# Performance work log

Measured on AMD Instinct MI355X. Metric: run time of the kernel, lower is better.

The kernel has to match this reference:

```python
import jax, jax.numpy as jnp
import numpy as np

B, SORB, H, L = 32768, 64, 256, 2


def setup_inputs() -> dict:
    key = jax.random.key(0)
    ks = jax.random.split(key, 11)
    s = 1.0 / np.sqrt(H)

    def u(k, shape):
        return jax.random.uniform(k, shape, jnp.float32, -s, s)

    return {
        "x": jax.random.randint(ks[0], (B, SORB), 0, 2).astype(jnp.int32),
        # PyTorch GRU params, gate order (r, z, n); layer 0 input_size=2, layer 1 input_size=H
        "w_ih0": u(ks[1], (3 * H, 2)), "w_hh0": u(ks[2], (3 * H, H)),
        "b_ih0": u(ks[3], (3 * H,)), "b_hh0": u(ks[4], (3 * H,)),
        "w_ih1": u(ks[5], (3 * H, H)), "w_hh1": u(ks[6], (3 * H, H)),
        "b_ih1": u(ks[7], (3 * H,)), "b_hh1": u(ks[8], (3 * H,)),
        "w_amp": u(ks[9], (2, H)), "b_amp": u(ks[10], (2,)),
    }


def _gru_cell(x, h, w_ih, w_hh, b_ih, b_hh):
    # PyTorch GRUCell math, gates in (r, z, n) order
    gi = x @ w_ih.T + b_ih
    gh = h @ w_hh.T + b_hh
    ir, iz, i_n = jnp.split(gi, 3, axis=-1)
    hr, hz, h_n = jnp.split(gh, 3, axis=-1)
    r = jax.nn.sigmoid(ir + hr)
    z = jax.nn.sigmoid(iz + hz)
    n = jnp.tanh(i_n + r * h_n)
    return (1.0 - z) * n + z * h


def reference(x, w_ih0, w_hh0, b_ih0, b_hh0, w_ih1, w_hh1, b_ih1, b_hh1, w_amp, b_amp):
    bits = x  # [B, SORB], values in {0,1} (equals ((+-1)+1)/2 of original input)
    nb = bits.shape[0]
    layer_params = [(w_ih0, w_hh0, b_ih0, b_hh0), (w_ih1, w_hh1, b_ih1, b_hh1)]

    def stacked(inp, h):  # h: [L, B, H]
        hs = []
        for l, (wi, wh, bi, bh) in enumerate(layer_params):
            hl = _gru_cell(inp, h[l], wi, wh, bi, bh)
            hs.append(hl)
            inp = hl
        return inp, jnp.stack(hs)

    h0 = jnp.zeros((L, nb, H), jnp.float32)
    # priming step with zero input (x0 = zeros(nbatch,1,2))
    _, h = stacked(jnp.zeros((nb, 2), jnp.float32), h0)

    def step(h, b_t):  # b_t: [B]
        onehot = jax.nn.one_hot(b_t, 2, dtype=jnp.float32)
        y, h = stacked(onehot, h)
        amp = jax.nn.softmax(y @ w_amp.T + b_amp, axis=1)  # [B, 2]
        p = jnp.sum(amp * onehot, axis=1)  # conditional prob of the sampled bit
        return h, p

    _, probs = jax.lax.scan(step, h, bits.T)  # probs: [SORB, B]
    return jnp.sqrt(jnp.prod(probs, axis=0))  # wavefunction amplitude, [B]
```

## Files before the change

### kernel.cpp

```cpp
#include <hip/hip_runtime.h>

typedef _Float16 f16;
typedef _Float16 f16x8 __attribute__((ext_vector_type(8)));
typedef float f32x4 __attribute__((ext_vector_type(4)));

#define H_    256
#define TB_   64
#define NT_   1024
#define SORB_ 64
#define SLOT_ 8192

#define MFMA16(a, b, c) __builtin_amdgcn_mfma_f32_16x16x32_f16((a), (b), (c), 0, 0, 0)
#define UNR _Pragma("unroll")

__device__ __forceinline__ float sigm(float v) {
  return __builtin_amdgcn_rcpf(1.0f + __builtin_amdgcn_exp2f(v * -1.442695040888963f));
}
__device__ __forceinline__ float tanh_fast(float v) {
  float a = fabsf(v);
  float e = __builtin_amdgcn_exp2f(a * -2.885390081777927f);
  float t = (1.0f - e) * __builtin_amdgcn_rcpf(1.0f + e);
  return copysignf(t, v);
}
__device__ __forceinline__ int lswz(int lrow, int col) {
  return lrow * H_ + (col ^ ((lrow & 7) << 3));
}

__global__ void wcvt(const float* __restrict__ a, const float* __restrict__ b,
                     const float* __restrict__ c, f16* __restrict__ o) {
  int i = blockIdx.x * 256 + threadIdx.x;
  const int n = 768 * 256;
  if (i < n) {
    o[i]         = (f16)a[i];
    o[n + i]     = (f16)b[i];
    o[2 * n + i] = (f16)c[i];
  }
}

__global__ __launch_bounds__(NT_, 4) void rnnwf(
    const int* __restrict__ x,
    const float* __restrict__ w_ih0, const float* __restrict__ b_ih0,
    const float* __restrict__ b_hh0, const float* __restrict__ b_ih1,
    const float* __restrict__ b_hh1, const float* __restrict__ w_amp,
    const float* __restrict__ b_amp, const f16* __restrict__ W16,
    float* __restrict__ out)
{
  __shared__ __align__(16) f16 hall[6 * SLOT_];
  __shared__ float wampL[512];
  __shared__ unsigned short bitsL[TB_ * 4];
  __shared__ unsigned long long bitsT[SORB_];

  const int tid  = threadIdx.x;
  const int wave = tid >> 6;
  const int lane = tid & 63;
  const int l15  = lane & 15;
  const int lg   = lane >> 4;
  const int lg4  = lg << 2;
  const int col  = wave * 16 + l15;
  const int rowbase = blockIdx.x * TB_;

  for (int j = tid; j < 512; j += NT_) wampL[j] = w_amp[j];
  if (tid < 256) {
    int row = tid >> 2, q = tid & 3;
    const int* xp = x + (size_t)(rowbase + row) * SORB_ + q * 16;
    unsigned m = 0;
    #pragma unroll
    for (int i = 0; i < 16; ++i) m |= (unsigned)(xp[i] & 1) << i;
    bitsL[row * 4 + q] = (unsigned short)m;
  }
  for (int i = tid; i < 6 * SLOT_; i += NT_) hall[i] = (f16)0.f;

  const float baseR = b_ih0[col]       + b_hh0[col];
  const float baseZ = b_ih0[256 + col] + b_hh0[256 + col];
  const float baseN = b_ih0[512 + col];
  const float wR0 = w_ih0[2 * col + 0],         wR1 = w_ih0[2 * col + 1];
  const float wZ0 = w_ih0[2 * (256 + col) + 0], wZ1 = w_ih0[2 * (256 + col) + 1];
  const float wN0 = w_ih0[2 * (512 + col) + 0], wN1 = w_ih0[2 * (512 + col) + 1];
  const float sumR0 = baseR + wR0, dR = wR1 - wR0;
  const float sumZ0 = baseZ + wZ0, dZ = wZ1 - wZ0;
  const float sumN0 = baseN + wN0, dN = wN1 - wN0;
  const float bhh0n_c = b_hh0[512 + col];
  const float b1r_c   = b_ih1[col]       + b_hh1[col];
  const float b1z_c   = b_ih1[256 + col] + b_hh1[256 + col];
  const float b1ni_c  = b_ih1[512 + col];
  const float b1nh_c  = b_hh1[512 + col];
  const float ba0 = b_amp[0], ba1 = b_amp[1];
  __syncthreads();

  if (tid < SORB_) {
    unsigned long long mk = 0ull;
    const int q = tid >> 4, sh = tid & 15;
    #pragma unroll 4
    for (int r = 0; r < TB_; ++r)
      mk |= (unsigned long long)((bitsL[r * 4 + q] >> sh) & 1) << r;
    bitsT[tid] = mk;
  }
  __syncthreads();

  float prob = 1.0f;
  const f16* Wih1 = W16 + 768 * 256;
  const f16* Whh1 = W16 + 2 * 768 * 256;
  const f16* p0base = W16  + col * 256;
  const f16* pibase = Wih1 + col * 256;
  const f16* phbase = Whh1 + col * 256;

  const int hrow = tid >> 4;
  const int hsh  = hrow & 31;
  const bool hhi = hrow >= 32;

  int pa = 0, pb = 2 * SLOT_, pc = 4 * SLOT_;

  for (int t = -1; t < SORB_; ++t) {
    unsigned lo32 = 0u, hi32 = 0u;
    if (t >= 0) {
      unsigned long long mk = bitsT[t];
      lo32 = (unsigned)mk; hi32 = (unsigned)(mk >> 32);
    }

    {
      f32x4 aR[4], aZ[4], aN[4];
      UNR for (int m = 0; m < 4; ++m) { aR[m] = (f32x4){0,0,0,0}; aZ[m] = aR[m]; aN[m] = aR[m]; }
      #pragma unroll 2
      for (int kt = 0; kt < 8; ++kt) {
        const int k0 = kt * 32 + lg * 8;
        f16x8 Br = *(const f16x8*)(p0base + k0);
        f16x8 Bz = *(const f16x8*)(p0base + 65536 + k0);
        f16x8 Bn = *(const f16x8*)(p0base + 131072 + k0);
        UNR for (int m = 0; m < 4; ++m) {
          f16x8 A = *(const f16x8*)&hall[pa + (m >> 1) * SLOT_ + lswz((m & 1) * 16 + l15, k0)];
          aR[m] = MFMA16(A, Br, aR[m]);
          aZ[m] = MFMA16(A, Bz, aZ[m]);
          aN[m] = MFMA16(A, Bn, aN[m]);
        }
      }
      if (t >= 0) {
        UNR for (int m = 0; m < 4; ++m) {
          const unsigned hsel = (m < 2) ? lo32 : hi32;
          UNR for (int e = 0; e < 4; ++e) {
            const int lrow = (m & 1) * 16 + lg4 + e;
            float fb = (float)((hsel >> ((m & 1) * 16 + lg4 + e)) & 1u);
            float giR = fmaf(fb, dR, sumR0);
            float giZ = fmaf(fb, dZ, sumZ0);
            float giN = fmaf(fb, dN, sumN0);
            float r  = sigm(aR[m][e] + giR);
            float z  = sigm(aZ[m][e] + giZ);
            float n  = tanh_fast(giN + r * (aN[m][e] + bhh0n_c));
            float ho = (float)hall[pa + (m >> 1) * SLOT_ + lswz(lrow, col)];
            hall[pc + (m >> 1) * SLOT_ + lswz(lrow, col)] = (f16)((1.0f - z) * n + z * ho);
          }
        }
      } else {
        UNR for (int m = 0; m < 4; ++m) {
          UNR for (int e = 0; e < 4; ++e) {
            const int lrow = (m & 1) * 16 + lg4 + e;
            float r  = sigm(aR[m][e] + baseR);
            float z  = sigm(aZ[m][e] + baseZ);
            float n  = tanh_fast(baseN + r * (aN[m][e] + bhh0n_c));
            float ho = (float)hall[pa + (m >> 1) * SLOT_ + lswz(lrow, col)];
            hall[pc + (m >> 1) * SLOT_ + lswz(lrow, col)] = (f16)((1.0f - z) * n + z * ho);
          }
        }
      }
    }
    __syncthreads();

    {
      f32x4 aR[4], aZ[4];
      UNR for (int m = 0; m < 4; ++m) { aR[m] = (f32x4){0,0,0,0}; aZ[m] = aR[m]; }
      #pragma unroll 2
      for (int kt = 0; kt < 8; ++kt) {
        const int k0 = kt * 32 + lg * 8;
        f16x8 BiR = *(const f16x8*)(pibase + k0);
        f16x8 BiZ = *(const f16x8*)(pibase + 65536 + k0);
        f16x8 BhR = *(const f16x8*)(phbase + k0);
        f16x8 BhZ = *(const f16x8*)(phbase + 65536 + k0);
        UNR for (int m = 0; m < 4; ++m) {
          f16x8 A0 = *(const f16x8*)&hall[pc + (m >> 1) * SLOT_ + lswz((m & 1) * 16 + l15, k0)];
          f16x8 A1 = *(const f16x8*)&hall[pb + (m >> 1) * SLOT_ + lswz((m & 1) * 16 + l15, k0)];
          aR[m] = MFMA16(A0, BiR, aR[m]);  aR[m] = MFMA16(A1, BhR, aR[m]);
          aZ[m] = MFMA16(A0, BiZ, aZ[m]);  aZ[m] = MFMA16(A1, BhZ, aZ[m]);
        }
      }
      f32x4 rv[4], zv[4];
      UNR for (int m = 0; m < 4; ++m)
        UNR for (int e = 0; e < 4; ++e) {
          rv[m][e] = sigm(aR[m][e] + b1r_c);
          zv[m][e] = sigm(aZ[m][e] + b1z_c);
        }
      f32x4 aNi[4], aNh[4];
      UNR for (int m = 0; m < 4; ++m) { aNi[m] = (f32x4){0,0,0,0}; aNh[m] = aNi[m]; }
      #pragma unroll 2
      for (int kt = 0; kt < 8; ++kt) {
        const int k0 = kt * 32 + lg * 8;
        f16x8 BiN = *(const f16x8*)(pibase + 131072 + k0);
        f16x8 BhN = *(const f16x8*)(phbase + 131072 + k0);
        UNR for (int m = 0; m < 4; ++m) {
          f16x8 A0 = *(const f16x8*)&hall[pc + (m >> 1) * SLOT_ + lswz((m & 1) * 16 + l15, k0)];
          f16x8 A1 = *(const f16x8*)&hall[pb + (m >> 1) * SLOT_ + lswz((m & 1) * 16 + l15, k0)];
          aNi[m] = MFMA16(A0, BiN, aNi[m]);
          aNh[m] = MFMA16(A1, BhN, aNh[m]);
        }
      }
      UNR for (int m = 0; m < 4; ++m) {
        UNR for (int e = 0; e < 4; ++e) {
          const int lrow = (m & 1) * 16 + lg4 + e;
          float n  = tanh_fast(aNi[m][e] + b1ni_c + rv[m][e] * (aNh[m][e] + b1nh_c));
          float z  = zv[m][e];
          float ho = (float)hall[pb + (m >> 1) * SLOT_ + lswz(lrow, col)];
          hall[pa + (m >> 1) * SLOT_ + lswz(lrow, col)] = (f16)((1.0f - z) * n + z * ho);
        }
      }
    }
    __syncthreads();

    if (t >= 0) {
      const int t16 = tid & 15;
      float d0 = 0.f, d1 = 0.f;
      #pragma unroll
      for (int j = 0; j < 2; ++j) {
        const int k0 = t16 * 16 + j * 8;
        f16x8 hv = *(const f16x8*)&hall[pa + (hrow >> 5) * SLOT_ + lswz(hrow & 31, k0)];
        f32x4 w0a = *(const f32x4*)&wampL[k0];
        f32x4 w0b = *(const f32x4*)&wampL[k0 + 4];
        f32x4 w1a = *(const f32x4*)&wampL[256 + k0];
        f32x4 w1b = *(const f32x4*)&wampL[256 + k0 + 4];
        #pragma unroll
        for (int i = 0; i < 4; ++i) {
          float hfa = (float)hv[i], hfb = (float)hv[4 + i];
          d0 = fmaf(hfa, w0a[i], d0); d0 = fmaf(hfb, w0b[i], d0);
          d1 = fmaf(hfa, w1a[i], d1); d1 = fmaf(hfb, w1b[i], d1);
        }
      }
      d0 += __shfl_xor(d0, 1); d0 += __shfl_xor(d0, 2);
      d0 += __shfl_xor(d0, 4); d0 += __shfl_xor(d0, 8);
      d1 += __shfl_xor(d1, 1); d1 += __shfl_xor(d1, 2);
      d1 += __shfl_xor(d1, 4); d1 += __shfl_xor(d1, 8);
      const unsigned hm = hhi ? hi32 : lo32;
      const int bit = (hm >> hsh) & 1;
      float diff = (d0 + ba0) - (d1 + ba1);
      if (bit) diff = -diff;
      prob *= __builtin_amdgcn_rcpf(1.0f + __builtin_amdgcn_exp2f(diff * -1.442695040888963f));
    }

    int tmp = pa; pa = pc; pc = pb; pb = tmp;
  }

  if ((tid & 15) == 0) out[rowbase + (tid >> 4)] = sqrtf(prob);
}

extern "C" void kernel_launch(void* const* d_in, const int* in_sizes, int n_in,
                              void* d_out, int out_size, void* d_ws, size_t ws_size,
                              hipStream_t stream) {
  const int*   x     = (const int*)d_in[0];
  const float* w_ih0 = (const float*)d_in[1];
  const float* w_hh0 = (const float*)d_in[2];
  const float* b_ih0 = (const float*)d_in[3];
  const float* b_hh0 = (const float*)d_in[4];
  const float* w_ih1 = (const float*)d_in[5];
  const float* w_hh1 = (const float*)d_in[6];
  const float* b_ih1 = (const float*)d_in[7];
  const float* b_hh1 = (const float*)d_in[8];
  const float* w_amp = (const float*)d_in[9];
  const float* b_amp = (const float*)d_in[10];
  (void)in_sizes; (void)n_in; (void)out_size; (void)ws_size;

  f16* W16 = (f16*)d_ws;
  hipLaunchKernelGGL(wcvt, dim3(768), dim3(256), 0, stream, w_hh0, w_ih1, w_hh1, W16);
  hipLaunchKernelGGL(rnnwf, dim3(32768 / TB_), dim3(NT_), 0, stream,
                     x, w_ih0, b_ih0, b_hh0, b_ih1, b_hh1, w_amp, b_amp, W16,
                     (float*)d_out);
}
```

Baseline: 5.107 ms.

## Halve rows per block and have each wave compute two column tiles

Cuts the batch tile from 64 to 32 rows and the block from 1024 to 512 threads, so each wave now handles two 16-column tiles (col and col+128) over 32 rows instead of one tile over 64 rows. Hidden-state LDS shrinks by half, and the per-row bit masks are now held in registers, read straight from packed shorts, instead of being transposed into a shared bitsT table. The aim is more resident blocks per CU and smaller LDS and sync scope. In exchange each B-fragment of the weights is reused across fewer A-rows, which doubles global or L2 weight traffic per row.

```diff
diff --git a/kernel.cpp b/kernel.cpp
--- a/kernel.cpp
+++ b/kernel.cpp
@@ -5,8 +5,9 @@
 typedef float f32x4 __attribute__((ext_vector_type(4)));
 
 #define H_    256
-#define TB_   64
-#define NT_   1024
+#define TB_   32
+#define NT_   512
+#define NWG_  1024
 #define SORB_ 64
 #define SLOT_ 8192
 
@@ -45,10 +46,8 @@
     const float* __restrict__ b_amp, const f16* __restrict__ W16,
     float* __restrict__ out)
 {
-  __shared__ __align__(16) f16 hall[6 * SLOT_];
+  __shared__ __align__(16) f16 hall[3 * SLOT_];
   __shared__ float wampL[512];
-  __shared__ unsigned short bitsL[TB_ * 4];
-  __shared__ unsigned long long bitsT[SORB_];
 
   const int tid  = threadIdx.x;
   const int wave = tid >> 6;
@@ -56,170 +55,164 @@
   const int l15  = lane & 15;
   const int lg   = lane >> 4;
   const int lg4  = lg << 2;
-  const int col  = wave * 16 + l15;
+  const int colA = wave * 16 + l15;
+  const int colB = colA + 128;
   const int rowbase = blockIdx.x * TB_;
 
   for (int j = tid; j < 512; j += NT_) wampL[j] = w_amp[j];
-  if (tid < 256) {
-    int row = tid >> 2, q = tid & 3;
-    const int* xp = x + (size_t)(rowbase + row) * SORB_ + q * 16;
+  if (tid < TB_ * 4) {
+    const int* xp = x + (size_t)(rowbase + (tid >> 2)) * SORB_ + (tid & 3) * 16;
     unsigned m = 0;
     #pragma unroll
     for (int i = 0; i < 16; ++i) m |= (unsigned)(xp[i] & 1) << i;
-    bitsL[row * 4 + q] = (unsigned short)m;
-  }
-  for (int i = tid; i < 6 * SLOT_; i += NT_) hall[i] = (f16)0.f;
-
-  const float baseR = b_ih0[col]       + b_hh0[col];
-  const float baseZ = b_ih0[256 + col] + b_hh0[256 + col];
-  const float baseN = b_ih0[512 + col];
-  const float wR0 = w_ih0[2 * col + 0],         wR1 = w_ih0[2 * col + 1];
-  const float wZ0 = w_ih0[2 * (256 + col) + 0], wZ1 = w_ih0[2 * (256 + col) + 1];
-  const float wN0 = w_ih0[2 * (512 + col) + 0], wN1 = w_ih0[2 * (512 + col) + 1];
-  const float sumR0 = baseR + wR0, dR = wR1 - wR0;
-  const float sumZ0 = baseZ + wZ0, dZ = wZ1 - wZ0;
-  const float sumN0 = baseN + wN0, dN = wN1 - wN0;
-  const float bhh0n_c = b_hh0[512 + col];
-  const float b1r_c   = b_ih1[col]       + b_hh1[col];
-  const float b1z_c   = b_ih1[256 + col] + b_hh1[256 + col];
-  const float b1ni_c  = b_ih1[512 + col];
-  const float b1nh_c  = b_hh1[512 + col];
+    ((unsigned short*)hall)[tid] = (unsigned short)m;
+  }
+  __syncthreads();
+  unsigned long long mk[8];
+  UNR for (int m = 0; m < 2; ++m)
+    UNR for (int e = 0; e < 4; ++e)
+      mk[m * 4 + e] = ((const unsigned long long*)hall)[m * 16 + lg4 + e];
+  const unsigned long long hmk = ((const unsigned long long*)hall)[tid >> 4];
+  __syncthreads();
+  for (int i = tid; i < 3 * SLOT_; i += NT_) hall[i] = (f16)0.f;
+
+  float sumR0[2], dR[2], sumZ0[2], dZ[2], sumN0[2], dN[2], bhh0n_c[2];
+  float b1r_c[2], b1z_c[2], b1ni_c[2], b1nh_c[2];
+  UNR for (int nt = 0; nt < 2; ++nt) {
+    const int c = nt ? colB : colA;
+    const float baseR = b_ih0[c] + b_hh0[c];
+    const float baseZ = b_ih0[256 + c] + b_hh0[256 + c];
+    const float baseN = b_ih0[512 + c];
+    sumR0[nt] = baseR + w_ih0[2 * c + 0];           dR[nt] = w_ih0[2 * c + 1] - w_ih0[2 * c + 0];
+    sumZ0[nt] = baseZ + w_ih0[2 * (256 + c) + 0];   dZ[nt] = w_ih0[2 * (256 + c) + 1] - w_ih0[2 * (256 + c) + 0];
+    sumN0[nt] = baseN + w_ih0[2 * (512 + c) + 0];   dN[nt] = w_ih0[2 * (512 + c) + 1] - w_ih0[2 * (512 + c) + 0];
+    bhh0n_c[nt] = b_hh0[512 + c];
+    b1r_c[nt]  = b_ih1[c] + b_hh1[c];
+    b1z_c[nt]  = b_ih1[256 + c] + b_hh1[256 + c];
+    b1ni_c[nt] = b_ih1[512 + c];
+    b1nh_c[nt] = b_hh1[512 + c];
+  }
   const float ba0 = b_amp[0], ba1 = b_amp[1];
-  __syncthreads();
-
-  if (tid < SORB_) {
-    unsigned long long mk = 0ull;
-    const int q = tid >> 4, sh = tid & 15;
-    #pragma unroll 4
-    for (int r = 0; r < TB_; ++r)
-      mk |= (unsigned long long)((bitsL[r * 4 + q] >> sh) & 1) << r;
-    bitsT[tid] = mk;
-  }
   __syncthreads();
 
   float prob = 1.0f;
   const f16* Wih1 = W16 + 768 * 256;
   const f16* Whh1 = W16 + 2 * 768 * 256;
-  const f16* p0base = W16  + col * 256;
-  const f16* pibase = Wih1 + col * 256;
-  const f16* phbase = Whh1 + col * 256;
-
   const int hrow = tid >> 4;
-  const int hsh  = hrow & 31;
-  const bool hhi = hrow >= 32;
-
-  int pa = 0, pb = 2 * SLOT_, pc = 4 * SLOT_;
+  const int t16  = tid & 15;
+
+  int pa = 0, pb = SLOT_, pc = 2 * SLOT_;
 
   for (int t = -1; t < SORB_; ++t) {
-    unsigned lo32 = 0u, hi32 = 0u;
-    if (t >= 0) {
-      unsigned long long mk = bitsT[t];
-      lo32 = (unsigned)mk; hi32 = (unsigned)(mk >> 32);
-    }
-
-    {
-      f32x4 aR[4], aZ[4], aN[4];
-      UNR for (int m = 0; m < 4; ++m) { aR[m] = (f32x4){0,0,0,0}; aZ[m] = aR[m]; aN[m] = aR[m]; }
+    UNR for (int nt = 0; nt < 2; ++nt) {
+      const int c = nt ? colB : colA;
+      const f16* p0 = W16 + c * 256;
+      f32x4 aR[2], aZ[2], aN[2];
+      UNR for (int m = 0; m < 2; ++m) { aR[m] = (f32x4){0,0,0,0}; aZ[m] = aR[m]; aN[m] = aR[m]; }
       #pragma unroll 2
       for (int kt = 0; kt < 8; ++kt) {
         const int k0 = kt * 32 + lg * 8;
-        f16x8 Br = *(const f16x8*)(p0base + k0);
-        f16x8 Bz = *(const f16x8*)(p0base + 65536 + k0);
-        f16x8 Bn = *(const f16x8*)(p0base + 131072 + k0);
-        UNR for (int m = 0; m < 4; ++m) {
-          f16x8 A = *(const f16x8*)&hall[pa + (m >> 1) * SLOT_ + lswz((m & 1) * 16 + l15, k0)];
+        f16x8 Br = *(const f16x8*)(p0 + k0);
+        f16x8 Bz = *(const f16x8*)(p0 + 65536 + k0);
+        f16x8 Bn = *(const f16x8*)(p0 + 131072 + k0);
+        UNR for (int m = 0; m < 2; ++m) {
+          f16x8 A = *(const f16x8*)&hall[pa + lswz(m * 16 + l15, k0)];
           aR[m] = MFMA16(A, Br, aR[m]);
           aZ[m] = MFMA16(A, Bz, aZ[m]);
           aN[m] = MFMA16(A, Bn, aN[m]);
         }
       }
       if (t >= 0) {
-        UNR for (int m = 0; m < 4; ++m) {
-          const unsigned hsel = (m < 2) ? lo32 : hi32;
+        UNR for (int m = 0; m < 2; ++m) {
           UNR for (int e = 0; e < 4; ++e) {
-            const int lrow = (m & 1) * 16 + lg4 + e;
-            float fb = (float)((hsel >> ((m & 1) * 16 + lg4 + e)) & 1u);
-            float giR = fmaf(fb, dR, sumR0);
-            float giZ = fmaf(fb, dZ, sumZ0);
-            float giN = fmaf(fb, dN, sumN0);
+            const int lrow = m * 16 + lg4 + e;
+            float fb = (float)((unsigned)(mk[m * 4 + e] >> t) & 1u);
+            float giR = fmaf(fb, dR[nt], sumR0[nt]);
+            float giZ = fmaf(fb, dZ[nt], sumZ0[nt]);
+            float giN = fmaf(fb, dN[nt], sumN0[nt]);
             float r  = sigm(aR[m][e] + giR);
             float z  = sigm(aZ[m][e] + giZ);
-            float n  = tanh_fast(giN + r * (aN[m][e] + bhh0n_c));
-            float ho = (float)hall[pa + (m >> 1) * SLOT_ + lswz(lrow, col)];
-            hall[pc + (m >> 1) * SLOT_ + lswz(lrow, col)] = (f16)((1.0f - z) * n + z * ho);
+            float n  = tanh_fast(giN + r * (aN[m][e] + bhh0n_c[nt]));
+            float ho = (float)hall[pa + lswz(lrow, c)];
+            hall[pc + lswz(lrow, c)] = (f16)((1.0f - z) * n + z * ho);
           }
         }
       } else {
-        UNR for (int m = 0; m < 4; ++m) {
+        const float pR = b_ih0[c] + b_hh0[c];
+        const float pZ = b_ih0[256 + c] + b_hh0[256 + c];
+        const float pN = b_ih0[512 + c];
+        UNR for (int m = 0; m < 2; ++m) {
           UNR for (int e = 0; e < 4; ++e) {
-            const int lrow = (m & 1) * 16 + lg4 + e;
-            float r  = sigm(aR[m][e] + baseR);
-            float z  = sigm(aZ[m][e] + baseZ);
-            float n  = tanh_fast(baseN + r * (aN[m][e] + bhh0n_c));
-            float ho = (float)hall[pa + (m >> 1) * SLOT_ + lswz(lrow, col)];
-            hall[pc + (m >> 1) * SLOT_ + lswz(lrow, col)] = (f16)((1.0f - z) * n + z * ho);
+            const int lrow = m * 16 + lg4 + e;
+            float r  = sigm(aR[m][e] + pR);
+            float z  = sigm(aZ[m][e] + pZ);
+            float n  = tanh_fast(pN + r * (aN[m][e] + bhh0n_c[nt]));
+            float ho = (float)hall[pa + lswz(lrow, c)];
+            hall[pc + lswz(lrow, c)] = (f16)((1.0f - z) * n + z * ho);
           }
         }
       }
     }
     __syncthreads();
 
-    {
-      f32x4 aR[4], aZ[4];
-      UNR for (int m = 0; m < 4; ++m) { aR[m] = (f32x4){0,0,0,0}; aZ[m] = aR[m]; }
+    UNR for (int nt = 0; nt < 2; ++nt) {
+      const int c = nt ? colB : colA;
+      const f16* pi = Wih1 + c * 256;
+      const f16* ph = Whh1 + c * 256;
+      f32x4 aR[2], aZ[2];
+      UNR for (int m = 0; m < 2; ++m) { aR[m] = (f32x4){0,0,0,0}; aZ[m] = aR[m]; }
       #pragma unroll 2
       for (int kt = 0; kt < 8; ++kt) {
         const int k0 = kt * 32 + lg * 8;
-        f16x8 BiR = *(const f16x8*)(pibase + k0);
-        f16x8 BiZ = *(const f16x8*)(pibase + 65536 + k0);
-        f16x8 BhR = *(const f16x8*)(phbase + k0);
-        f16x8 BhZ = *(const f16x8*)(phbase + 65536 + k0);
-        UNR for (int m = 0; m < 4; ++m) {
-          f16x8 A0 = *(const f16x8*)&hall[pc + (m >> 1) * SLOT_ + lswz((m & 1) * 16 + l15, k0)];
-          f16x8 A1 = *(const f16x8*)&hall[pb + (m >> 1) * SLOT_ + lswz((m & 1) * 16 + l15, k0)];
+        f16x8 BiR = *(const f16x8*)(pi + k0);
+        f16x8 BiZ = *(const f16x8*)(pi + 65536 + k0);
+        f16x8 BhR = *(const f16x8*)(ph + k0);
+        f16x8 BhZ = *(const f16x8*)(ph + 65536 + k0);
+        UNR for (int m = 0; m < 2; ++m) {
+          f16x8 A0 = *(const f16x8*)&hall[pc + lswz(m * 16 + l15, k0)];
+          f16x8 A1 = *(const f16x8*)&hall[pb + lswz(m * 16 + l15, k0)];
           aR[m] = MFMA16(A0, BiR, aR[m]);  aR[m] = MFMA16(A1, BhR, aR[m]);
           aZ[m] = MFMA16(A0, BiZ, aZ[m]);  aZ[m] = MFMA16(A1, BhZ, aZ[m]);
         }
       }
-      f32x4 rv[4], zv[4];
-      UNR for (int m = 0; m < 4; ++m)
+      f32x4 rv[2], zv[2];
+      UNR for (int m = 0; m < 2; ++m)
         UNR for (int e = 0; e < 4; ++e) {
-          rv[m][e] = sigm(aR[m][e] + b1r_c);
-          zv[m][e] = sigm(aZ[m][e] + b1z_c);
-        }
-      f32x4 aNi[4], aNh[4];
-      UNR for (int m = 0; m < 4; ++m) { aNi[m] = (f32x4){0,0,0,0}; aNh[m] = aNi[m]; }
+          rv[m][e] = sigm(aR[m][e] + b1r_c[nt]);
+          zv[m][e] = sigm(aZ[m][e] + b1z_c[nt]);
+        }
+      f32x4 aNi[2], aNh[2];
+      UNR for (int m = 0; m < 2; ++m) { aNi[m] = (f32x4){0,0,0,0}; aNh[m] = aNi[m]; }
       #pragma unroll 2
       for (int kt = 0; kt < 8; ++kt) {
         const int k0 = kt * 32 + lg * 8;
-        f16x8 BiN = *(const f16x8*)(pibase + 131072 + k0);
-        f16x8 BhN = *(const f16x8*)(phbase + 131072 + k0);
-        UNR for (int m = 0; m < 4; ++m) {
-          f16x8 A0 = *(const f16x8*)&hall[pc + (m >> 1) * SLOT_ + lswz((m & 1) * 16 + l15, k0)];
-          f16x8 A1 = *(const f16x8*)&hall[pb + (m >> 1) * SLOT_ + lswz((m & 1) * 16 + l15, k0)];
+        f16x8 BiN = *(const f16x8*)(pi + 131072 + k0);
+        f16x8 BhN = *(const f16x8*)(ph + 131072 + k0);
+        UNR for (int m = 0; m < 2; ++m) {
+          f16x8 A0 = *(const f16x8*)&hall[pc + lswz(m * 16 + l15, k0)];
+          f16x8 A1 = *(const f16x8*)&hall[pb + lswz(m * 16 + l15, k0)];
           aNi[m] = MFMA16(A0, BiN, aNi[m]);
           aNh[m] = MFMA16(A1, BhN, aNh[m]);
         }
       }
-      UNR for (int m = 0; m < 4; ++m) {
+      UNR for (int m = 0; m < 2; ++m) {
         UNR for (int e = 0; e < 4; ++e) {
-          const int lrow = (m & 1) * 16 + lg4 + e;
-          float n  = tanh_fast(aNi[m][e] + b1ni_c + rv[m][e] * (aNh[m][e] + b1nh_c));
+          const int lrow = m * 16 + lg4 + e;
+          float n  = tanh_fast(aNi[m][e] + b1ni_c[nt] + rv[m][e] * (aNh[m][e] + b1nh_c[nt]));
           float z  = zv[m][e];
-          float ho = (float)hall[pb + (m >> 1) * SLOT_ + lswz(lrow, col)];
-          hall[pa + (m >> 1) * SLOT_ + lswz(lrow, col)] = (f16)((1.0f - z) * n + z * ho);
+          float ho = (float)hall[pb + lswz(lrow, c)];
+          hall[pa + lswz(lrow, c)] = (f16)((1.0f - z) * n + z * ho);
         }
       }
     }
     __syncthreads();
 
     if (t >= 0) {
-      const int t16 = tid & 15;
       float d0 = 0.f, d1 = 0.f;
       #pragma unroll
       for (int j = 0; j < 2; ++j) {
         const int k0 = t16 * 16 + j * 8;
-        f16x8 hv = *(const f16x8*)&hall[pa + (hrow >> 5) * SLOT_ + lswz(hrow & 31, k0)];
+        f16x8 hv = *(const f16x8*)&hall[pa + lswz(hrow, k0)];
         f32x4 w0a = *(const f32x4*)&wampL[k0];
         f32x4 w0b = *(const f32x4*)&wampL[k0 + 4];
         f32x4 w1a = *(const f32x4*)&wampL[256 + k0];
@@ -235,8 +228,7 @@
       d0 += __shfl_xor(d0, 4); d0 += __shfl_xor(d0, 8);
       d1 += __shfl_xor(d1, 1); d1 += __shfl_xor(d1, 2);
       d1 += __shfl_xor(d1, 4); d1 += __shfl_xor(d1, 8);
-      const unsigned hm = hhi ? hi32 : lo32;
-      const int bit = (hm >> hsh) & 1;
+      const int bit = (unsigned)(hmk >> t) & 1u;
       float diff = (d0 + ba0) - (d1 + ba1);
       if (bit) diff = -diff;
       prob *= __builtin_amdgcn_rcpf(1.0f + __builtin_amdgcn_exp2f(diff * -1.442695040888963f));
@@ -245,7 +237,7 @@
     int tmp = pa; pa = pc; pc = pb; pb = tmp;
   }
 
-  if ((tid & 15) == 0) out[rowbase + (tid >> 4)] = sqrtf(prob);
+  if (t16 == 0) out[rowbase + hrow] = sqrtf(prob);
 }
 
 extern "C" void kernel_launch(void* const* d_in, const int* in_sizes, int n_in,
@@ -266,7 +258,7 @@
 
   f16* W16 = (f16*)d_ws;
   hipLaunchKernelGGL(wcvt, dim3(768), dim3(256), 0, stream, w_hh0, w_ih1, w_hh1, W16);
-  hipLaunchKernelGGL(rnnwf, dim3(32768 / TB_), dim3(NT_), 0, stream,
+  hipLaunchKernelGGL(rnnwf, dim3(NWG_), dim3(NT_), 0, stream,
                      x, w_ih0, b_ih0, b_hh0, b_ih1, b_hh1, w_amp, b_amp, W16,
                      (float*)d_out);
 }
```

After: 8.445 ms. 1.65x slower.

## Software-pipeline GRU layers across timesteps with one barrier per step

Applied to the files above, without the earlier changes.

Restructures the time loop so that layer 0 at step tau and layer 1 at step tau-1 run in the same iteration, each reading double-buffered hidden states. The amplitude softmax for step tau-2 is folded in as well, and the shared A0 fragment is loaded once for both layer-0 gates and layer-1 input gates. This cuts the barriers per step from two to one and interleaves independent MFMA work. In exchange it grows LDS to eight slots, which may lower occupancy, and adds an epilogue iteration for the final step.

```diff
diff --git a/kernel.cpp b/kernel.cpp
--- a/kernel.cpp
+++ b/kernel.cpp
@@ -45,9 +45,9 @@
     const float* __restrict__ b_amp, const f16* __restrict__ W16,
     float* __restrict__ out)
 {
-  __shared__ __align__(16) f16 hall[6 * SLOT_];
+  __shared__ __align__(16) f16 hall[8 * SLOT_];
   __shared__ float wampL[512];
-  __shared__ unsigned short bitsL[TB_ * 4];
+  __shared__ __align__(8) unsigned short bitsL[TB_ * 4];
   __shared__ unsigned long long bitsT[SORB_];
 
   const int tid  = threadIdx.x;
@@ -60,25 +60,33 @@
   const int rowbase = blockIdx.x * TB_;
 
   for (int j = tid; j < 512; j += NT_) wampL[j] = w_amp[j];
-  if (tid < 256) {
-    int row = tid >> 2, q = tid & 3;
-    const int* xp = x + (size_t)(rowbase + row) * SORB_ + q * 16;
+  if (tid < TB_ * 4) {
+    const int* xp = x + (size_t)(rowbase + (tid >> 2)) * SORB_ + (tid & 3) * 16;
     unsigned m = 0;
     #pragma unroll
     for (int i = 0; i < 16; ++i) m |= (unsigned)(xp[i] & 1) << i;
-    bitsL[row * 4 + q] = (unsigned short)m;
-  }
-  for (int i = tid; i < 6 * SLOT_; i += NT_) hall[i] = (f16)0.f;
+    bitsL[tid] = (unsigned short)m;
+  }
+  for (int i = tid; i < 8 * SLOT_; i += NT_) hall[i] = (f16)0.f;
+  __syncthreads();
+  if (tid < SORB_) {
+    unsigned long long mkk = 0ull;
+    const int q = tid >> 4, sh = tid & 15;
+    #pragma unroll 4
+    for (int r = 0; r < TB_; ++r)
+      mkk |= (unsigned long long)((bitsL[r * 4 + q] >> sh) & 1) << r;
+    bitsT[tid] = mkk;
+  }
+  const int hrow = tid >> 4;
+  const int t16  = tid & 15;
+  const unsigned long long hmk = ((const unsigned long long*)bitsL)[hrow];
 
   const float baseR = b_ih0[col]       + b_hh0[col];
   const float baseZ = b_ih0[256 + col] + b_hh0[256 + col];
   const float baseN = b_ih0[512 + col];
-  const float wR0 = w_ih0[2 * col + 0],         wR1 = w_ih0[2 * col + 1];
-  const float wZ0 = w_ih0[2 * (256 + col) + 0], wZ1 = w_ih0[2 * (256 + col) + 1];
-  const float wN0 = w_ih0[2 * (512 + col) + 0], wN1 = w_ih0[2 * (512 + col) + 1];
-  const float sumR0 = baseR + wR0, dR = wR1 - wR0;
-  const float sumZ0 = baseZ + wZ0, dZ = wZ1 - wZ0;
-  const float sumN0 = baseN + wN0, dN = wN1 - wN0;
+  const float sumR0 = baseR + w_ih0[2 * col + 0],         dR = w_ih0[2 * col + 1] - w_ih0[2 * col + 0];
+  const float sumZ0 = baseZ + w_ih0[2 * (256 + col) + 0], dZ = w_ih0[2 * (256 + col) + 1] - w_ih0[2 * (256 + col) + 0];
+  const float sumN0 = baseN + w_ih0[2 * (512 + col) + 0], dN = w_ih0[2 * (512 + col) + 1] - w_ih0[2 * (512 + col) + 0];
   const float bhh0n_c = b_hh0[512 + col];
   const float b1r_c   = b_ih1[col]       + b_hh1[col];
   const float b1z_c   = b_ih1[256 + col] + b_hh1[256 + col];
@@ -87,53 +95,87 @@
   const float ba0 = b_amp[0], ba1 = b_amp[1];
   __syncthreads();
 
-  if (tid < SORB_) {
-    unsigned long long mk = 0ull;
-    const int q = tid >> 4, sh = tid & 15;
-    #pragma unroll 4
-    for (int r = 0; r < TB_; ++r)
-      mk |= (unsigned long long)((bitsL[r * 4 + q] >> sh) & 1) << r;
-    bitsT[tid] = mk;
-  }
-  __syncthreads();
-
   float prob = 1.0f;
-  const f16* Wih1 = W16 + 768 * 256;
-  const f16* Whh1 = W16 + 2 * 768 * 256;
-  const f16* p0base = W16  + col * 256;
-  const f16* pibase = Wih1 + col * 256;
-  const f16* phbase = Whh1 + col * 256;
-
-  const int hrow = tid >> 4;
-  const int hsh  = hrow & 31;
-  const bool hhi = hrow >= 32;
-
-  int pa = 0, pb = 2 * SLOT_, pc = 4 * SLOT_;
-
-  for (int t = -1; t < SORB_; ++t) {
+  const f16* p0base = W16 + col * 256;
+  const f16* pibase = W16 + 768 * 256 + col * 256;
+  const f16* phbase = W16 + 2 * 768 * 256 + col * 256;
+
+  for (int tau = -1; tau <= 64; ++tau) {
+    const int h0r = ((tau + 1) & 1) * (2 * SLOT_);
+    const int h0w = (tau & 1) * (2 * SLOT_);
+    const int h1r = 4 * SLOT_ + ((tau + 1) & 1) * (2 * SLOT_);
+    const int h1w = 4 * SLOT_ + (tau & 1) * (2 * SLOT_);
+    const bool doS = (tau < 64), doT = (tau >= 0);
+
     unsigned lo32 = 0u, hi32 = 0u;
-    if (t >= 0) {
-      unsigned long long mk = bitsT[t];
-      lo32 = (unsigned)mk; hi32 = (unsigned)(mk >> 32);
-    }
-
-    {
-      f32x4 aR[4], aZ[4], aN[4];
-      UNR for (int m = 0; m < 4; ++m) { aR[m] = (f32x4){0,0,0,0}; aZ[m] = aR[m]; aN[m] = aR[m]; }
+    if (tau >= 0 && tau < 64) {
+      unsigned long long mkk = bitsT[tau];
+      lo32 = (unsigned)mkk; hi32 = (unsigned)(mkk >> 32);
+    }
+
+    f32x4 aR0[4], aZ0[4], aN0[4], tR[4], tZ[4];
+    UNR for (int m = 0; m < 4; ++m) {
+      aR0[m] = (f32x4){0,0,0,0}; aZ0[m] = aR0[m]; aN0[m] = aR0[m];
+      tR[m] = aR0[m]; tZ[m] = aR0[m];
+    }
+    #pragma unroll 2
+    for (int kt = 0; kt < 8; ++kt) {
+      const int k0 = kt * 32 + lg * 8;
+      f16x8 A0[4];
+      UNR for (int m = 0; m < 4; ++m)
+        A0[m] = *(const f16x8*)&hall[h0r + (m >> 1) * SLOT_ + lswz((m & 1) * 16 + l15, k0)];
+      if (doS) {
+        f16x8 Br = *(const f16x8*)(p0base + k0);
+        f16x8 Bz = *(const f16x8*)(p0base + 65536 + k0);
+        f16x8 Bn = *(const f16x8*)(p0base + 131072 + k0);
+        UNR for (int m = 0; m < 4; ++m) {
+          aR0[m] = MFMA16(A0[m], Br, aR0[m]);
+          aZ0[m] = MFMA16(A0[m], Bz, aZ0[m]);
+          aN0[m] = MFMA16(A0[m], Bn, aN0[m]);
+        }
+      }
+      if (doT) {
+        f16x8 BiR = *(const f16x8*)(pibase + k0);
+        f16x8 BiZ = *(const f16x8*)(pibase + 65536 + k0);
+        f16x8 BhR = *(const f16x8*)(phbase + k0);
+        f16x8 BhZ = *(const f16x8*)(phbase + 65536 + k0);
+        f16x8 A1[4];
+        UNR for (int m = 0; m < 4; ++m)
+          A1[m] = *(const f16x8*)&hall[h1r + (m >> 1) * SLOT_ + lswz((m & 1) * 16 + l15, k0)];
+        UNR for (int m = 0; m < 4; ++m) {
+          tR[m] = MFMA16(A0[m], BiR, tR[m]);  tR[m] = MFMA16(A1[m], BhR, tR[m]);
+          tZ[m] = MFMA16(A0[m], BiZ, tZ[m]);  tZ[m] = MFMA16(A1[m], BhZ, tZ[m]);
+        }
+      }
+    }
+    f32x4 rv[4], zv[4];
+    if (doT) {
+      UNR for (int m = 0; m < 4; ++m)
+        UNR for (int e = 0; e < 4; ++e) {
+          rv[m][e] = sigm(tR[m][e] + b1r_c);
+          zv[m][e] = sigm(tZ[m][e] + b1z_c);
+        }
+    }
+
+    f32x4 tNi[4], tNh[4];
+    UNR for (int m = 0; m < 4; ++m) { tNi[m] = (f32x4){0,0,0,0}; tNh[m] = tNi[m]; }
+    if (doT) {
       #pragma unroll 2
       for (int kt = 0; kt < 8; ++kt) {
         const int k0 = kt * 32 + lg * 8;
-        f16x8 Br = *(const f16x8*)(p0base + k0);
-        f16x8 Bz = *(const f16x8*)(p0base + 65536 + k0);
-        f16x8 Bn = *(const f16x8*)(p0base + 131072 + k0);
-        UNR for (int m = 0; m < 4; ++m) {
-          f16x8 A = *(const f16x8*)&hall[pa + (m >> 1) * SLOT_ + lswz((m & 1) * 16 + l15, k0)];
-          aR[m] = MFMA16(A, Br, aR[m]);
-          aZ[m] = MFMA16(A, Bz, aZ[m]);
-          aN[m] = MFMA16(A, Bn, aN[m]);
-        }
-      }
-      if (t >= 0) {
+        f16x8 BiN = *(const f16x8*)(pibase + 131072 + k0);
+        f16x8 BhN = *(const f16x8*)(phbase + 131072 + k0);
+        UNR for (int m = 0; m < 4; ++m) {
+          f16x8 A0 = *(const f16x8*)&hall[h0r + (m >> 1) * SLOT_ + lswz((m & 1) * 16 + l15, k0)];
+          f16x8 A1 = *(const f16x8*)&hall[h1r + (m >> 1) * SLOT_ + lswz((m & 1) * 16 + l15, k0)];
+          tNi[m] = MFMA16(A0, BiN, tNi[m]);
+          tNh[m] = MFMA16(A1, BhN, tNh[m]);
+        }
+      }
+    }
+
+    if (doS) {
+      if (tau >= 0) {
         UNR for (int m = 0; m < 4; ++m) {
           const unsigned hsel = (m < 2) ? lo32 : hi32;
           UNR for (int e = 0; e < 4; ++e) {
@@ -142,84 +184,44 @@
             float giR = fmaf(fb, dR, sumR0);
             float giZ = fmaf(fb, dZ, sumZ0);
             float giN = fmaf(fb, dN, sumN0);
-            float r  = sigm(aR[m][e] + giR);
-            float z  = sigm(aZ[m][e] + giZ);
-            float n  = tanh_fast(giN + r * (aN[m][e] + bhh0n_c));
-            float ho = (float)hall[pa + (m >> 1) * SLOT_ + lswz(lrow, col)];
-            hall[pc + (m >> 1) * SLOT_ + lswz(lrow, col)] = (f16)((1.0f - z) * n + z * ho);
+            float r  = sigm(aR0[m][e] + giR);
+            float z  = sigm(aZ0[m][e] + giZ);
+            float n  = tanh_fast(giN + r * (aN0[m][e] + bhh0n_c));
+            float ho = (float)hall[h0r + (m >> 1) * SLOT_ + lswz(lrow, col)];
+            hall[h0w + (m >> 1) * SLOT_ + lswz(lrow, col)] = (f16)((1.0f - z) * n + z * ho);
           }
         }
       } else {
         UNR for (int m = 0; m < 4; ++m) {
           UNR for (int e = 0; e < 4; ++e) {
             const int lrow = (m & 1) * 16 + lg4 + e;
-            float r  = sigm(aR[m][e] + baseR);
-            float z  = sigm(aZ[m][e] + baseZ);
-            float n  = tanh_fast(baseN + r * (aN[m][e] + bhh0n_c));
-            float ho = (float)hall[pa + (m >> 1) * SLOT_ + lswz(lrow, col)];
-            hall[pc + (m >> 1) * SLOT_ + lswz(lrow, col)] = (f16)((1.0f - z) * n + z * ho);
+            float r  = sigm(aR0[m][e] + baseR);
+            float z  = sigm(aZ0[m][e] + baseZ);
+            float n  = tanh_fast(baseN + r * (aN0[m][e] + bhh0n_c));
+            float ho = (float)hall[h0r + (m >> 1) * SLOT_ + lswz(lrow, col)];
+            hall[h0w + (m >> 1) * SLOT_ + lswz(lrow, col)] = (f16)((1.0f - z) * n + z * ho);
           }
         }
       }
     }
-    __syncthreads();
-
-    {
-      f32x4 aR[4], aZ[4];
-      UNR for (int m = 0; m < 4; ++m) { aR[m] = (f32x4){0,0,0,0}; aZ[m] = aR[m]; }
-      #pragma unroll 2
-      for (int kt = 0; kt < 8; ++kt) {
-        const int k0 = kt * 32 + lg * 8;
-        f16x8 BiR = *(const f16x8*)(pibase + k0);
-        f16x8 BiZ = *(const f16x8*)(pibase + 65536 + k0);
-        f16x8 BhR = *(const f16x8*)(phbase + k0);
-        f16x8 BhZ = *(const f16x8*)(phbase + 65536 + k0);
-        UNR for (int m = 0; m < 4; ++m) {
-          f16x8 A0 = *(const f16x8*)&hall[pc + (m >> 1) * SLOT_ + lswz((m & 1) * 16 + l15, k0)];
-          f16x8 A1 = *(const f16x8*)&hall[pb + (m >> 1) * SLOT_ + lswz((m & 1) * 16 + l15, k0)];
-          aR[m] = MFMA16(A0, BiR, aR[m]);  aR[m] = MFMA16(A1, BhR, aR[m]);
-          aZ[m] = MFMA16(A0, BiZ, aZ[m]);  aZ[m] = MFMA16(A1, BhZ, aZ[m]);
-        }
-      }
-      f32x4 rv[4], zv[4];
-      UNR for (int m = 0; m < 4; ++m)
-        UNR for (int e = 0; e < 4; ++e) {
-          rv[m][e] = sigm(aR[m][e] + b1r_c);
-          zv[m][e] = sigm(aZ[m][e] + b1z_c);
-        }
-      f32x4 aNi[4], aNh[4];
-      UNR for (int m = 0; m < 4; ++m) { aNi[m] = (f32x4){0,0,0,0}; aNh[m] = aNi[m]; }
-      #pragma unroll 2
-      for (int kt = 0; kt < 8; ++kt) {
-        const int k0 = kt * 32 + lg * 8;
-        f16x8 BiN = *(const f16x8*)(pibase + 131072 + k0);
-        f16x8 BhN = *(const f16x8*)(phbase + 131072 + k0);
-        UNR for (int m = 0; m < 4; ++m) {
-          f16x8 A0 = *(const f16x8*)&hall[pc + (m >> 1) * SLOT_ + lswz((m & 1) * 16 + l15, k0)];
-          f16x8 A1 = *(const f16x8*)&hall[pb + (m >> 1) * SLOT_ + lswz((m & 1) * 16 + l15, k0)];
-          aNi[m] = MFMA16(A0, BiN, aNi[m]);
-          aNh[m] = MFMA16(A1, BhN, aNh[m]);
-        }
-      }
+    if (doT) {
       UNR for (int m = 0; m < 4; ++m) {
         UNR for (int e = 0; e < 4; ++e) {
           const int lrow = (m & 1) * 16 + lg4 + e;
-          float n  = tanh_fast(aNi[m][e] + b1ni_c + rv[m][e] * (aNh[m][e] + b1nh_c));
+          float n  = tanh_fast(tNi[m][e] + b1ni_c + rv[m][e] * (tNh[m][e] + b1nh_c));
           float z  = zv[m][e];
-          float ho = (float)hall[pb + (m >> 1) * SLOT_ + lswz(lrow, col)];
-          hall[pa + (m >> 1) * SLOT_ + lswz(lrow, col)] = (f16)((1.0f - z) * n + z * ho);
-        }
-      }
-    }
-    __syncthreads();
-
-    if (t >= 0) {
-      const int t16 = tid & 15;
+          float ho = (float)hall[h1r + (m >> 1) * SLOT_ + lswz(lrow, col)];
+          hall[h1w + (m >> 1) * SLOT_ + lswz(lrow, col)] = (f16)((1.0f - z) * n + z * ho);
+        }
+      }
+    }
+    if (tau >= 2) {
+      const int t = tau - 2;
       float d0 = 0.f, d1 = 0.f;
       #pragma unroll
       for (int j = 0; j < 2; ++j) {
         const int k0 = t16 * 16 + j * 8;
-        f16x8 hv = *(const f16x8*)&hall[pa + (hrow >> 5) * SLOT_ + lswz(hrow & 31, k0)];
+        f16x8 hv = *(const f16x8*)&hall[h1r + (hrow >> 5) * SLOT_ + lswz(hrow & 31, k0)];
         f32x4 w0a = *(const f32x4*)&wampL[k0];
         f32x4 w0b = *(const f32x4*)&wampL[k0 + 4];
         f32x4 w1a = *(const f32x4*)&wampL[256 + k0];
@@ -235,17 +237,43 @@
       d0 += __shfl_xor(d0, 4); d0 += __shfl_xor(d0, 8);
       d1 += __shfl_xor(d1, 1); d1 += __shfl_xor(d1, 2);
       d1 += __shfl_xor(d1, 4); d1 += __shfl_xor(d1, 8);
-      const unsigned hm = hhi ? hi32 : lo32;
-      const int bit = (hm >> hsh) & 1;
+      const int bit = (unsigned)(hmk >> t) & 1u;
       float diff = (d0 + ba0) - (d1 + ba1);
       if (bit) diff = -diff;
       prob *= __builtin_amdgcn_rcpf(1.0f + __builtin_amdgcn_exp2f(diff * -1.442695040888963f));
     }
-
-    int tmp = pa; pa = pc; pc = pb; pb = tmp;
-  }
-
-  if ((tid & 15) == 0) out[rowbase + (tid >> 4)] = sqrtf(prob);
+    __syncthreads();
+  }
+
+  {
+    const int hb = 4 * SLOT_;
+    float d0 = 0.f, d1 = 0.f;
+    #pragma unroll
+    for (int j = 0; j < 2; ++j) {
+      const int k0 = t16 * 16 + j * 8;
+      f16x8 hv = *(const f16x8*)&hall[hb + (hrow >> 5) * SLOT_ + lswz(hrow & 31, k0)];
+      f32x4 w0a = *(const f32x4*)&wampL[k0];
+      f32x4 w0b = *(const f32x4*)&wampL[k0 + 4];
+      f32x4 w1a = *(const f32x4*)&wampL[256 + k0];
+      f32x4 w1b = *(const f32x4*)&wampL[256 + k0 + 4];
+      #pragma unroll
+      for (int i = 0; i < 4; ++i) {
+        float hfa = (float)hv[i], hfb = (float)hv[4 + i];
+        d0 = fmaf(hfa, w0a[i], d0); d0 = fmaf(hfb, w0b[i], d0);
+        d1 = fmaf(hfa, w1a[i], d1); d1 = fmaf(hfb, w1b[i], d1);
+      }
+    }
+    d0 += __shfl_xor(d0, 1); d0 += __shfl_xor(d0, 2);
+    d0 += __shfl_xor(d0, 4); d0 += __shfl_xor(d0, 8);
+    d1 += __shfl_xor(d1, 1); d1 += __shfl_xor(d1, 2);
+    d1 += __shfl_xor(d1, 4); d1 += __shfl_xor(d1, 8);
+    const int bit = (unsigned)(hmk >> 63) & 1u;
+    float diff = (d0 + ba0) - (d1 + ba1);
+    if (bit) diff = -diff;
+    prob *= __builtin_amdgcn_rcpf(1.0f + __builtin_amdgcn_exp2f(diff * -1.442695040888963f));
+  }
+
+  if (t16 == 0) out[rowbase + hrow] = sqrtf(prob);
 }
 
 extern "C" void kernel_launch(void* const* d_in, const int* in_sizes, int n_in,
```

Measured after the change: 5.883 ms. 15.2% more time.
